# Kernel tuning notes

Measured on AMD Instinct MI355X. Metric: run time of the kernel, lower is better.

The kernel has to match this reference:

```python
import jax, jax.numpy as jnp
import numpy as np

H = 16      # multiheads
DH = 64     # head_dim
NEG = 1e12  # mask constant from original code


def setup_inputs() -> dict:
    key = jax.random.key(0)
    ks = jax.random.split(key, 8)
    B, S, D = 8, 1024, 1024
    out_dim = H * DH
    glorot = lambda k, shape: jax.random.uniform(
        k, shape, jnp.float32, -1.0, 1.0) * np.sqrt(6.0 / (shape[0] + shape[1]))
    return {
        "Q_seq": jax.random.normal(ks[0], (B, S, D), jnp.float32),
        "K_seq": jax.random.normal(ks[1], (B, S, D), jnp.float32),
        "V_seq": jax.random.normal(ks[2], (B, S, D), jnp.float32),
        "Q_len": jax.random.randint(ks[3], (B, 1), 0, S, jnp.int32),
        "V_len": jax.random.randint(ks[4], (B, 1), 0, S, jnp.int32),
        "WQ": glorot(ks[5], (D, out_dim)),
        "WK": glorot(ks[6], (D, out_dim)),
        "WV": glorot(ks[7], (D, out_dim)),
    }


def reference(Q_seq, K_seq, V_seq, Q_len, V_len, WQ, WK, WV):
    B, Sq, _ = Q_seq.shape
    Sk = K_seq.shape[1]

    def proj(x, W):  # (B,S,D) -> (B,H,S,DH)
        return (x @ W).reshape(B, x.shape[1], H, DH).transpose(0, 2, 1, 3)

    q = proj(Q_seq, WQ)
    k = proj(K_seq, WK)
    v = proj(V_seq, WV)

    # scores: (B,H,Sq,Sk)
    A = jnp.einsum('bhqd,bhkd->bhqk', q, k) / jnp.sqrt(jnp.float32(DH))

    # key-side length mask (Mask mode='add'): positions >= V_len get -1e12
    kv_valid = (jnp.arange(Sk)[None, :] < V_len).astype(A.dtype)  # (B,Sk)
    A = A - (1.0 - kv_valid)[:, None, None, :] * NEG

    # causal (mask_right=True): upper triangle masked
    causal = jnp.tril(jnp.ones((Sq, Sk), dtype=A.dtype))
    A = A - (1.0 - causal)[None, None, :, :] * NEG

    A = jax.nn.softmax(A, axis=-1)

    O = jnp.einsum('bhqk,bhkd->bhqd', A, v)          # (B,H,Sq,DH)
    O = O.transpose(0, 2, 1, 3).reshape(B, Sq, H * DH)

    # query-side length mask (Mask mode='mul')
    q_valid = (jnp.arange(Sq)[None, :] < Q_len).astype(O.dtype)  # (B,Sq)
    return O * q_valid[:, :, None]
```

## Files before the change

kernel.cpp:

```cpp
#include <hip/hip_runtime.h>
#include <hip/hip_bf16.h>
#include <stdint.h>

#define H_ 16
#define DH_ 64
#define B_ 8
#define S_ 1024
#define D_ 1024

using bf16 = __hip_bfloat16;
typedef __attribute__((ext_vector_type(8))) short bfrag;
typedef __attribute__((ext_vector_type(4))) float facc;
typedef __attribute__((ext_vector_type(4))) float f4;

#define SWZ(r) ((((r) & 7) << 4) ^ (((r) & 8) << 3))
#define SWZP(r) ((((r) >> 1) & 3) << 4)

__device__ __forceinline__ int proj_len(int z, int Ql, int Vl) {
  if (z == 0) return Ql;
  if (z == 1) return Vl;
  return Vl ? Vl : min(Ql + 63, S_);
}

__global__ __launch_bounds__(256) void convert3_f32_bf16(const float* __restrict__ Q,
                                                         const float* __restrict__ K,
                                                         const float* __restrict__ V,
                                                         bf16* __restrict__ o0,
                                                         bf16* __restrict__ o1,
                                                         bf16* __restrict__ o2,
                                                         const int* __restrict__ Qlen,
                                                         const int* __restrict__ Vlen) {
  int z = blockIdx.z;
  int row = blockIdx.x * 2;
  int bb = row >> 10;
  int lrow = row & (S_ - 1);
  int len = proj_len(z, Qlen[bb], Vlen[bb]);
  if ((lrow & ~127) >= len) return;
  const float* in = (z == 0) ? Q : (z == 1) ? K : V;
  bf16* outb = (z == 0) ? o0 : (z == 1) ? o1 : o2;
  int i = blockIdx.x * 256 + threadIdx.x;
  f4 a = ((const f4*)in)[2 * i];
  f4 b = ((const f4*)in)[2 * i + 1];
  alignas(16) bf16 tmp[8];
#pragma unroll
  for (int j = 0; j < 4; ++j) tmp[j] = __float2bfloat16(a[j]);
#pragma unroll
  for (int j = 0; j < 4; ++j) tmp[4 + j] = __float2bfloat16(b[j]);
  *(bfrag*)&outb[8 * i] = *(const bfrag*)tmp;
}

__global__ __launch_bounds__(256) void transpose_w3(const float* __restrict__ WQ,
                                                    const float* __restrict__ WK,
                                                    const float* __restrict__ WV,
                                                    bf16* __restrict__ WT) {
  __shared__ bf16 tile[32][33];
  int z = blockIdx.z;
  const float* W = (z == 0) ? WQ : (z == 1) ? WK : WV;
  float scale = (z == 0) ? 0.125f * 1.44269504f : 1.0f;
  int tx = threadIdx.x & 31, ty = threadIdx.x >> 5;
  int bx = blockIdx.x, by = blockIdx.y;
#pragma unroll
  for (int i = 0; i < 4; ++i) {
    int kk = by * 32 + ty + 8 * i;
    int nn = bx * 32 + tx;
    tile[ty + 8 * i][tx] = __float2bfloat16(W[kk * D_ + nn] * scale);
  }
  __syncthreads();
#pragma unroll
  for (int i = 0; i < 4; ++i) {
    int nn = bx * 32 + ty + 8 * i;
    int kk = by * 32 + tx;
    WT[((size_t)z * 1024 + nn) * D_ + kk] = tile[tx][ty + 8 * i];
  }
}

__global__ __launch_bounds__(256) void proj_gemm(const bf16* __restrict__ A0,
                                                 const bf16* __restrict__ A1,
                                                 const bf16* __restrict__ A2,
                                                 const bf16* __restrict__ Bt,
                                                 bf16* __restrict__ qb,
                                                 bf16* __restrict__ kb,
                                                 bf16* __restrict__ vb,
                                                 const int* __restrict__ Qlen,
                                                 const int* __restrict__ Vlen,
                                                 int zbase) {
  __shared__ __align__(16) bf16 As[128][32];
  __shared__ __align__(16) bf16 Bs[128][32];
  int z = blockIdx.z + zbase;
  int m0 = blockIdx.x * 128;
  int bb = m0 >> 10;
  int len = proj_len(z, Qlen[bb], Vlen[bb]);
  if ((m0 & (S_ - 1)) >= len) return;
  const bf16* A = (z == 0) ? A0 : (z == 1) ? A1 : A2;
  bf16* outp = (z == 0) ? qb : (z == 1) ? kb : vb;
  int tid = threadIdx.x;
  int lane = tid & 63;
  int wave = tid >> 6;
  int n0 = blockIdx.y * 128;
  int nw = z * 1024 + n0;
  int wm = (wave >> 1) * 64;
  int wn = (wave & 1) * 64;
  int l15 = lane & 15, l4 = lane >> 4;
  int br = lane >> 2;
  int lc = ((lane & 3) ^ ((br >> 1) & 3)) * 8;

  facc acc[4][4] = {};

  for (int k0 = 0; k0 < D_; k0 += 32) {
    __syncthreads();
#pragma unroll
    for (int c = 0; c < 2; ++c) {
      int row = wave * 32 + c * 16;
      __builtin_amdgcn_global_load_lds(
          (const __attribute__((address_space(1))) void*)&A[(size_t)(m0 + row + br) * D_ + k0 + lc],
          (__attribute__((address_space(3))) void*)&As[row][0], 16, 0, 0);
      __builtin_amdgcn_global_load_lds(
          (const __attribute__((address_space(1))) void*)&Bt[(size_t)(nw + row + br) * D_ + k0 + lc],
          (__attribute__((address_space(3))) void*)&Bs[row][0], 16, 0, 0);
    }
    __syncthreads();
    bfrag af[4], bfr[4];
    const char* Ab = (const char*)&As[0][0];
    const char* Bb = (const char*)&Bs[0][0];
#pragma unroll
    for (int i = 0; i < 4; ++i) {
      int row = wm + i * 16 + l15;
      af[i] = *(const bfrag*)(Ab + row * 64 + ((l4 * 16) ^ SWZP(row)));
    }
#pragma unroll
    for (int j = 0; j < 4; ++j) {
      int row = wn + j * 16 + l15;
      bfr[j] = *(const bfrag*)(Bb + row * 64 + ((l4 * 16) ^ SWZP(row)));
    }
#pragma unroll
    for (int i = 0; i < 4; ++i)
#pragma unroll
      for (int j = 0; j < 4; ++j)
        acc[i][j] = __builtin_amdgcn_mfma_f32_16x16x32_bf16(af[i], bfr[j], acc[i][j], 0, 0, 0);
  }

  bool vmode = (z == 2);
#pragma unroll
  for (int i = 0; i < 4; ++i)
#pragma unroll
    for (int j = 0; j < 4; ++j)
#pragma unroll
      for (int r = 0; r < 4; ++r) {
        int gm = m0 + wm + i * 16 + l4 * 4 + r;
        int gn = n0 + wn + j * 16 + l15;
        int b = gm >> 10, s = gm & (S_ - 1);
        int h = gn >> 6, dh = gn & 63;
        bf16 val = __float2bfloat16(acc[i][j][r]);
        if (!vmode)
          outp[(((size_t)b * H_ + h) * S_ + s) * DH_ + dh] = val;
        else
          outp[(((size_t)b * H_ + h) * DH_ + dh) * S_ + s] = val;
      }
}

__global__ __launch_bounds__(256) void attn_fwd(const bf16* __restrict__ q,
                                                const bf16* __restrict__ k,
                                                const bf16* __restrict__ vT,
                                                const int* __restrict__ Qlen,
                                                const int* __restrict__ Vlen,
                                                float* __restrict__ out) {
  __shared__ __align__(16) bf16 Kt[2][64 * 64];
  __shared__ __align__(16) bf16 Vt[2][64 * 64];
  int tid = threadIdx.x, lane = tid & 63, wave = tid >> 6;
  int bid = blockIdx.x;
  int h = bid & 15, b = (bid >> 4) & 7;
  int qt = 15 - (bid >> 7);
  int q0b = qt * 64;
  int q0 = q0b + wave * 16;
  int Vl = Vlen[b], Ql = Qlen[b];
  int l15 = lane & 15, g = lane >> 4;
  int qrow = q0 + l15;

  if (q0b >= Ql) {
    f4 zz = {0.f, 0.f, 0.f, 0.f};
#pragma unroll
    for (int t = 0; t < 4; ++t)
      *(f4*)&out[((size_t)b * S_ + qrow) * (H_ * DH_) + h * DH_ + t * 16 + g * 4] = zz;
    return;
  }

  const bf16* qp = q + (size_t)(b * H_ + h) * S_ * DH_;
  const bf16* kp = k + (size_t)(b * H_ + h) * S_ * DH_;
  const bf16* vp = vT + (size_t)(b * H_ + h) * DH_ * S_;
  bool vzero = (Vl == 0);

  int jlim = vzero ? (qrow + 1) : min(qrow + 1, Vl);
  int wmin = vzero ? (q0 + 1) : min(q0 + 1, Vl);
  int wmax = vzero ? (q0 + 16) : min(q0 + 16, Vl);
  if (q0 >= Ql) wmax = 0;

  bfrag qf0 = *(const bfrag*)&qp[(q0 + l15) * DH_ + g * 8];
  bfrag qf1 = *(const bfrag*)&qp[(q0 + l15) * DH_ + 32 + g * 8];

  facc o[4] = {};
  float mrow = -1e30f, lrow = 0.f;

  int kendb = q0b + 64;
  if (!vzero) kendb = kendb < Vl ? kendb : Vl;
  int nblk = (kendb + 63) >> 6;

  int krow0 = 8 * (l15 >> 2) + (l15 & 3);
  int sr0 = wave * 16 + (lane >> 3);
  int sbb = (lane & 7) * 16;

  auto stage = [&](int buf, int kbase) {
    int r0 = sr0, r1 = sr0 + 8;
    const char* kg0 = (const char*)(kp + (size_t)(kbase + r0) * DH_) + (sbb ^ SWZ(r0));
    const char* kg1 = (const char*)(kp + (size_t)(kbase + r1) * DH_) + (sbb ^ SWZ(r1));
    const char* vg0 = (const char*)(vp + (size_t)r0 * S_ + kbase) + (sbb ^ SWZ(r0));
    const char* vg1 = (const char*)(vp + (size_t)r1 * S_ + kbase) + (sbb ^ SWZ(r1));
    char* kl = (char*)&Kt[buf][0] + wave * 2048;
    char* vl = (char*)&Vt[buf][0] + wave * 2048;
    __builtin_amdgcn_global_load_lds((const __attribute__((address_space(1))) void*)kg0,
        (__attribute__((address_space(3))) void*)kl, 16, 0, 0);
    __builtin_amdgcn_global_load_lds((const __attribute__((address_space(1))) void*)kg1,
        (__attribute__((address_space(3))) void*)(kl + 1024), 16, 0, 0);
    __builtin_amdgcn_global_load_lds((const __attribute__((address_space(1))) void*)vg0,
        (__attribute__((address_space(3))) void*)vl, 16, 0, 0);
    __builtin_amdgcn_global_load_lds((const __attribute__((address_space(1))) void*)vg1,
        (__attribute__((address_space(3))) void*)(vl + 1024), 16, 0, 0);
  };

  stage(0, 0);
  __syncthreads();

  for (int kb = 0; kb < nblk; ++kb) {
    int cur = kb & 1;
    int kbase = kb * 64;
    if (kb + 1 < nblk) stage(1 - cur, (kb + 1) * 64);

    if (kbase < wmax) {
      facc z[4] = {};
      if (!vzero) {
#pragma unroll
        for (int gg = 0; gg < 2; ++gg) {
          int ra = gg * 32 + krow0;
          int rb = ra + 4;
          const char* Kc = (const char*)&Kt[cur][0];
          bfrag a0 = *(const bfrag*)(Kc + ra * 128 + ((g * 16) ^ SWZ(ra)));
          bfrag a1 = *(const bfrag*)(Kc + ra * 128 + ((g * 16 + 64) ^ SWZ(ra)));
          z[2 * gg] = __builtin_amdgcn_mfma_f32_16x16x32_bf16(a0, qf0, z[2 * gg], 0, 0, 0);
          z[2 * gg] = __builtin_amdgcn_mfma_f32_16x16x32_bf16(a1, qf1, z[2 * gg], 0, 0, 0);
          bfrag a2 = *(const bfrag*)(Kc + rb * 128 + ((g * 16) ^ SWZ(rb)));
          bfrag a3 = *(const bfrag*)(Kc + rb * 128 + ((g * 16 + 64) ^ SWZ(rb)));
          z[2 * gg + 1] = __builtin_amdgcn_mfma_f32_16x16x32_bf16(a2, qf0, z[2 * gg + 1], 0, 0, 0);
          z[2 * gg + 1] = __builtin_amdgcn_mfma_f32_16x16x32_bf16(a3, qf1, z[2 * gg + 1], 0, 0, 0);
        }
      }

      float sv[16];
#pragma unroll
      for (int gg = 0; gg < 2; ++gg)
#pragma unroll
        for (int c = 0; c < 4; ++c) {
          sv[8 * gg + c] = z[2 * gg][c];
          sv[8 * gg + 4 + c] = z[2 * gg + 1][c];
        }
      if (kbase + 64 > wmin) {
#pragma unroll
        for (int gg = 0; gg < 2; ++gg)
#pragma unroll
          for (int c = 0; c < 8; ++c) {
            int j = kbase + 32 * gg + 8 * g + c;
            if (j >= jlim) sv[8 * gg + c] = -1e12f;
          }
      }

      float mxl = sv[0];
#pragma unroll
      for (int c = 1; c < 16; ++c) mxl = fmaxf(mxl, sv[c]);

      if (!__all(mxl <= mrow + 8.0f)) {
        float mx = fmaxf(mxl, __shfl_xor(mxl, 16, 64));
        mx = fmaxf(mx, __shfl_xor(mx, 32, 64));
        float nm = fmaxf(mrow, mx);
        float sc = exp2f(mrow - nm);
        lrow *= sc;
#pragma unroll
        for (int t = 0; t < 4; ++t)
#pragma unroll
          for (int r = 0; r < 4; ++r) o[t][r] *= sc;
        mrow = nm;
      }

      alignas(16) bf16 pb[16];
      float ss = 0.f;
#pragma unroll
      for (int c = 0; c < 16; ++c) {
        float pv = exp2f(sv[c] - mrow);
        ss += pv;
        pb[c] = __float2bfloat16(pv);
      }
      ss += __shfl_xor(ss, 16, 64);
      ss += __shfl_xor(ss, 32, 64);
      lrow += ss;

      bfrag pf0 = *(const bfrag*)&pb[0];
      bfrag pf1 = *(const bfrag*)&pb[8];
      const char* Vc = (const char*)&Vt[cur][0];
#pragma unroll
      for (int t = 0; t < 4; ++t) {
        int d = t * 16 + l15;
        bfrag vf0 = *(const bfrag*)(Vc + d * 128 + ((g * 16) ^ SWZ(d)));
        bfrag vf1 = *(const bfrag*)(Vc + d * 128 + ((g * 16 + 64) ^ SWZ(d)));
        o[t] = __builtin_amdgcn_mfma_f32_16x16x32_bf16(vf0, pf0, o[t], 0, 0, 0);
        o[t] = __builtin_amdgcn_mfma_f32_16x16x32_bf16(vf1, pf1, o[t], 0, 0, 0);
      }
    }

    __syncthreads();
  }

  float inv = 1.0f / lrow;
  if (qrow >= Ql) inv = 0.f;
#pragma unroll
  for (int t = 0; t < 4; ++t) {
    f4 ov;
#pragma unroll
    for (int r = 0; r < 4; ++r) ov[r] = o[t][r] * inv;
    *(f4*)&out[((size_t)b * S_ + qrow) * (H_ * DH_) + h * DH_ + t * 16 + g * 4] = ov;
  }
}

extern "C" void kernel_launch(void* const* d_in, const int* in_sizes, int n_in,
                              void* d_out, int out_size, void* d_ws, size_t ws_size,
                              hipStream_t stream) {
  const float* Qs = (const float*)d_in[0];
  const float* Ks = (const float*)d_in[1];
  const float* Vs = (const float*)d_in[2];
  const int* Qlen = (const int*)d_in[3];
  const int* Vlen = (const int*)d_in[4];
  const float* WQ = (const float*)d_in[5];
  const float* WK = (const float*)d_in[6];
  const float* WV = (const float*)d_in[7];
  float* out = (float*)d_out;

  char* ws = (char*)d_ws;
  const size_t MB = 1024 * 1024;
  bf16* wT = (bf16*)(ws + 0 * MB);
  dim3 tb(256);
  const int CVT_GRID = (B_ * S_ * D_) / (8 * 256);

  transpose_w3<<<dim3(32, 32, 3), tb, 0, stream>>>(WQ, WK, WV, wT);

  if (ws_size >= 102 * MB) {
    bf16* xc0 = (bf16*)(ws + 6 * MB);
    bf16* xc1 = (bf16*)(ws + 22 * MB);
    bf16* xc2 = (bf16*)(ws + 38 * MB);
    bf16* qb  = (bf16*)(ws + 54 * MB);
    bf16* kb  = (bf16*)(ws + 70 * MB);
    bf16* vb  = (bf16*)(ws + 86 * MB);
    convert3_f32_bf16<<<dim3(CVT_GRID, 1, 3), tb, 0, stream>>>(Qs, Ks, Vs, xc0, xc1, xc2,
                                                               Qlen, Vlen);
    proj_gemm<<<dim3(64, 8, 3), tb, 0, stream>>>(xc0, xc1, xc2, wT, qb, kb, vb,
                                                 Qlen, Vlen, 0);
    attn_fwd<<<dim3(B_ * H_ * (S_ / 64)), tb, 0, stream>>>(qb, kb, vb, Qlen, Vlen, out);
  } else {
    bf16* xc = (bf16*)(ws + 6 * MB);
    bf16* qb = (bf16*)(ws + 22 * MB);
    bf16* kb = (bf16*)(ws + 38 * MB);
    bf16* vb = (bf16*)(ws + 54 * MB);
    convert3_f32_bf16<<<dim3(CVT_GRID, 1, 1), tb, 0, stream>>>(Qs, Ks, Vs, xc, xc, xc,
                                                               Qlen, Vlen);
    proj_gemm<<<dim3(64, 8, 1), tb, 0, stream>>>(xc, xc, xc, wT, qb, kb, vb, Qlen, Vlen, 0);
    convert3_f32_bf16<<<dim3(CVT_GRID, 1, 1), tb, 0, stream>>>(Ks, Ks, Ks, xc, xc, xc,
                                                               Qlen, Vlen);
    proj_gemm<<<dim3(64, 8, 1), tb, 0, stream>>>(xc, xc, xc, wT, qb, kb, vb, Qlen, Vlen, 1);
    convert3_f32_bf16<<<dim3(CVT_GRID, 1, 1), tb, 0, stream>>>(Vs, Vs, Vs, xc, xc, xc,
                                                               Qlen, Vlen);
    proj_gemm<<<dim3(64, 8, 1), tb, 0, stream>>>(xc, xc, xc, wT, qb, kb, vb, Qlen, Vlen, 2);
    attn_fwd<<<dim3(B_ * H_ * (S_ / 64)), tb, 0, stream>>>(qb, kb, vb, Qlen, Vlen, out);
  }
}
```

Before: 122.9 us.

## Rewrite projection GEMM as 256x256 tiles with double-buffered async LDS pipeline

The projection GEMM grows from a 128x128 tile per 256-thread block to a 256x256 tile per 512-thread block with 8 waves. Each wave now owns 128x64 of output. The k-loop is now a double-buffered pipeline: global_load_lds prefetches of the next 64-wide k chunk are interleaved with MFMA on the current chunk, using explicit vmcnt waits, barriers and setprio. The aim is to raise arithmetic intensity and hide global-memory latency. The trade-offs are larger LDS use (128KB), higher register pressure from 32 accumulators, and coarser early-exit granularity for the length mask, so the convert kernel's skip check is widened to match.

```diff
diff --git a/kernel.cpp b/kernel.cpp
--- a/kernel.cpp
+++ b/kernel.cpp
@@ -35,7 +35,7 @@
   int bb = row >> 10;
   int lrow = row & (S_ - 1);
   int len = proj_len(z, Qlen[bb], Vlen[bb]);
-  if ((lrow & ~127) >= len) return;
+  if ((lrow & ~255) >= len) return;
   const float* in = (z == 0) ? Q : (z == 1) ? K : V;
   bf16* outb = (z == 0) ? o0 : (z == 1) ? o1 : o2;
   int i = blockIdx.x * 256 + threadIdx.x;
@@ -74,7 +74,7 @@
   }
 }
 
-__global__ __launch_bounds__(256) void proj_gemm(const bf16* __restrict__ A0,
+__global__ __launch_bounds__(512) void proj_gemm(const bf16* __restrict__ A0,
                                                  const bf16* __restrict__ A1,
                                                  const bf16* __restrict__ A2,
                                                  const bf16* __restrict__ Bt,
@@ -84,10 +84,10 @@
                                                  const int* __restrict__ Qlen,
                                                  const int* __restrict__ Vlen,
                                                  int zbase) {
-  __shared__ __align__(16) bf16 As[128][32];
-  __shared__ __align__(16) bf16 Bs[128][32];
+  __shared__ __align__(16) bf16 As[2][2][256][32];
+  __shared__ __align__(16) bf16 Bs[2][2][256][32];
   int z = blockIdx.z + zbase;
-  int m0 = blockIdx.x * 128;
+  int m0 = blockIdx.x * 256;
   int bb = m0 >> 10;
   int len = proj_len(z, Qlen[bb], Vlen[bb]);
   if ((m0 & (S_ - 1)) >= len) return;
@@ -95,62 +95,101 @@
   bf16* outp = (z == 0) ? qb : (z == 1) ? kb : vb;
   int tid = threadIdx.x;
   int lane = tid & 63;
-  int wave = tid >> 6;
-  int n0 = blockIdx.y * 128;
+  int wid = tid >> 6;
+  int n0 = blockIdx.y * 256;
   int nw = z * 1024 + n0;
-  int wm = (wave >> 1) * 64;
-  int wn = (wave & 1) * 64;
+  int wr = wid >> 2, wc = wid & 3;
   int l15 = lane & 15, l4 = lane >> 4;
-  int br = lane >> 2;
-  int lc = ((lane & 3) ^ ((br >> 1) & 3)) * 8;
-
-  facc acc[4][4] = {};
-
-  for (int k0 = 0; k0 < D_; k0 += 32) {
-    __syncthreads();
-#pragma unroll
-    for (int c = 0; c < 2; ++c) {
-      int row = wave * 32 + c * 16;
-      __builtin_amdgcn_global_load_lds(
-          (const __attribute__((address_space(1))) void*)&A[(size_t)(m0 + row + br) * D_ + k0 + lc],
-          (__attribute__((address_space(3))) void*)&As[row][0], 16, 0, 0);
-      __builtin_amdgcn_global_load_lds(
-          (const __attribute__((address_space(1))) void*)&Bt[(size_t)(nw + row + br) * D_ + k0 + lc],
-          (__attribute__((address_space(3))) void*)&Bs[row][0], 16, 0, 0);
+  int srow0 = tid >> 2;
+  int sslot = (tid & 3) * 16;
+
+  facc acc[8][4] = {};
+
+  auto stageA = [&](int buf, int ch, int kt) {
+#pragma unroll
+    for (int l = 0; l < 2; ++l) {
+      int row = l * 128 + srow0;
+      const char* src = (const char*)&A[(size_t)(m0 + row) * D_] + kt * 128 + ch * 64 +
+                        (sslot ^ SWZP(row));
+      char* dst = (char*)&As[buf][ch][0][0] + l * 8192 + wid * 1024;
+      __builtin_amdgcn_global_load_lds((const __attribute__((address_space(1))) void*)src,
+                                       (__attribute__((address_space(3))) void*)dst, 16, 0, 0);
     }
-    __syncthreads();
-    bfrag af[4], bfr[4];
-    const char* Ab = (const char*)&As[0][0];
-    const char* Bb = (const char*)&Bs[0][0];
-#pragma unroll
-    for (int i = 0; i < 4; ++i) {
-      int row = wm + i * 16 + l15;
-      af[i] = *(const bfrag*)(Ab + row * 64 + ((l4 * 16) ^ SWZP(row)));
+  };
+  auto stageB = [&](int buf, int ch, int kt) {
+#pragma unroll
+    for (int l = 0; l < 2; ++l) {
+      int row = l * 128 + srow0;
+      const char* src = (const char*)&Bt[(size_t)(nw + row) * D_] + kt * 128 + ch * 64 +
+                        (sslot ^ SWZP(row));
+      char* dst = (char*)&Bs[buf][ch][0][0] + l * 8192 + wid * 1024;
+      __builtin_amdgcn_global_load_lds((const __attribute__((address_space(1))) void*)src,
+                                       (__attribute__((address_space(3))) void*)dst, 16, 0, 0);
     }
-#pragma unroll
-    for (int j = 0; j < 4; ++j) {
-      int row = wn + j * 16 + l15;
-      bfr[j] = *(const bfrag*)(Bb + row * 64 + ((l4 * 16) ^ SWZP(row)));
+  };
+
+  stageA(0, 0, 0); stageB(0, 0, 0); stageA(0, 1, 0); stageB(0, 1, 0);
+  asm volatile("s_waitcnt vmcnt(0)" ::: "memory");
+  __builtin_amdgcn_s_barrier();
+
+  for (int c = 0; c < 16; ++c) {
+    int cur = c & 1;
+    const char* Ab = (const char*)&As[cur][0][0][0];
+    const char* Bb = (const char*)&Bs[cur][0][0][0];
+    bool last = (c == 15);
+#pragma unroll
+    for (int q = 0; q < 4; ++q) {
+      const int ks = q >> 1, mg = q & 1;
+      bfrag af[4], bfr[4];
+#pragma unroll
+      for (int i = 0; i < 4; ++i) {
+        int row = wr * 128 + (mg * 4 + i) * 16 + l15;
+        af[i] = *(const bfrag*)(Ab + ks * 16384 + row * 64 + ((l4 * 16) ^ SWZP(row)));
+      }
+#pragma unroll
+      for (int j = 0; j < 4; ++j) {
+        int row = wc * 64 + j * 16 + l15;
+        bfr[j] = *(const bfrag*)(Bb + ks * 16384 + row * 64 + ((l4 * 16) ^ SWZP(row)));
+      }
+      if (!last) {
+        if (q == 0) stageA(cur ^ 1, 0, c + 1);
+        else if (q == 1) stageB(cur ^ 1, 0, c + 1);
+        else if (q == 2) stageA(cur ^ 1, 1, c + 1);
+        else stageB(cur ^ 1, 1, c + 1);
+      }
+      if (q == 1) {
+        if (last) asm volatile("s_waitcnt vmcnt(0)" ::: "memory");
+        else      asm volatile("s_waitcnt vmcnt(4)" ::: "memory");
+      } else if (q == 3 && !last) {
+        asm volatile("s_waitcnt vmcnt(4)" ::: "memory");
+      }
+      __builtin_amdgcn_s_barrier();
+      asm volatile("s_waitcnt lgkmcnt(0)" ::: "memory");
+      __builtin_amdgcn_sched_barrier(0);
+      __builtin_amdgcn_s_setprio(1);
+#pragma unroll
+      for (int i = 0; i < 4; ++i)
+#pragma unroll
+        for (int j = 0; j < 4; ++j)
+          acc[mg * 4 + i][j] =
+              __builtin_amdgcn_mfma_f32_16x16x32_bf16(af[i], bfr[j], acc[mg * 4 + i][j], 0, 0, 0);
+      __builtin_amdgcn_s_setprio(0);
+      __builtin_amdgcn_s_barrier();
     }
-#pragma unroll
-    for (int i = 0; i < 4; ++i)
-#pragma unroll
-      for (int j = 0; j < 4; ++j)
-        acc[i][j] = __builtin_amdgcn_mfma_f32_16x16x32_bf16(af[i], bfr[j], acc[i][j], 0, 0, 0);
   }
 
   bool vmode = (z == 2);
 #pragma unroll
-  for (int i = 0; i < 4; ++i)
-#pragma unroll
-    for (int j = 0; j < 4; ++j)
+  for (int mf = 0; mf < 8; ++mf)
+#pragma unroll
+    for (int nf = 0; nf < 4; ++nf)
 #pragma unroll
       for (int r = 0; r < 4; ++r) {
-        int gm = m0 + wm + i * 16 + l4 * 4 + r;
-        int gn = n0 + wn + j * 16 + l15;
+        int gm = m0 + wr * 128 + mf * 16 + l4 * 4 + r;
+        int gn = n0 + wc * 64 + nf * 16 + l15;
         int b = gm >> 10, s = gm & (S_ - 1);
         int h = gn >> 6, dh = gn & 63;
-        bf16 val = __float2bfloat16(acc[i][j][r]);
+        bf16 val = __float2bfloat16(acc[mf][nf][r]);
         if (!vmode)
           outp[(((size_t)b * H_ + h) * S_ + s) * DH_ + dh] = val;
         else
@@ -343,7 +382,7 @@
   char* ws = (char*)d_ws;
   const size_t MB = 1024 * 1024;
   bf16* wT = (bf16*)(ws + 0 * MB);
-  dim3 tb(256);
+  dim3 tb(256), tb2(512);
   const int CVT_GRID = (B_ * S_ * D_) / (8 * 256);
 
   transpose_w3<<<dim3(32, 32, 3), tb, 0, stream>>>(WQ, WK, WV, wT);
@@ -357,8 +396,8 @@
     bf16* vb  = (bf16*)(ws + 86 * MB);
     convert3_f32_bf16<<<dim3(CVT_GRID, 1, 3), tb, 0, stream>>>(Qs, Ks, Vs, xc0, xc1, xc2,
                                                                Qlen, Vlen);
-    proj_gemm<<<dim3(64, 8, 3), tb, 0, stream>>>(xc0, xc1, xc2, wT, qb, kb, vb,
-                                                 Qlen, Vlen, 0);
+    proj_gemm<<<dim3(32, 4, 3), tb2, 0, stream>>>(xc0, xc1, xc2, wT, qb, kb, vb,
+                                                  Qlen, Vlen, 0);
     attn_fwd<<<dim3(B_ * H_ * (S_ / 64)), tb, 0, stream>>>(qb, kb, vb, Qlen, Vlen, out);
   } else {
     bf16* xc = (bf16*)(ws + 6 * MB);
@@ -367,13 +406,13 @@
     bf16* vb = (bf16*)(ws + 54 * MB);
     convert3_f32_bf16<<<dim3(CVT_GRID, 1, 1), tb, 0, stream>>>(Qs, Ks, Vs, xc, xc, xc,
                                                                Qlen, Vlen);
-    proj_gemm<<<dim3(64, 8, 1), tb, 0, stream>>>(xc, xc, xc, wT, qb, kb, vb, Qlen, Vlen, 0);
+    proj_gemm<<<dim3(32, 4, 1), tb2, 0, stream>>>(xc, xc, xc, wT, qb, kb, vb, Qlen, Vlen, 0);
     convert3_f32_bf16<<<dim3(CVT_GRID, 1, 1), tb, 0, stream>>>(Ks, Ks, Ks, xc, xc, xc,
                                                                Qlen, Vlen);
-    proj_gemm<<<dim3(64, 8, 1), tb, 0, stream>>>(xc, xc, xc, wT, qb, kb, vb, Qlen, Vlen, 1);
+    proj_gemm<<<dim3(32, 4, 1), tb2, 0, stream>>>(xc, xc, xc, wT, qb, kb, vb, Qlen, Vlen, 1);
     convert3_f32_bf16<<<dim3(CVT_GRID, 1, 1), tb, 0, stream>>>(Vs, Vs, Vs, xc, xc, xc,
                                                                Qlen, Vlen);
-    proj_gemm<<<dim3(64, 8, 1), tb, 0, stream>>>(xc, xc, xc, wT, qb, kb, vb, Qlen, Vlen, 2);
+    proj_gemm<<<dim3(32, 4, 1), tb2, 0, stream>>>(xc, xc, xc, wT, qb, kb, vb, Qlen, Vlen, 2);
     attn_fwd<<<dim3(B_ * H_ * (S_ / 64)), tb, 0, stream>>>(qb, kb, vb, Qlen, Vlen, out);
   }
 }
```

Result: slower. 145.7 us (+18.5%).
